# Performance work log

Measured on AMD Instinct MI355X. Metric: run time of the kernel, lower is better.

## Reference

```python
import jax, jax.numpy as jnp
import numpy as np
import math

N = 50000          # number of nodes
K = 32             # fixed neighbor-list degree
D_IN = 256
D_OUT = 256
TPERC = 0.45


def setup_inputs() -> dict:
    key = jax.random.key(0)
    k1, k2, k3 = jax.random.split(key, 3)
    x = jax.random.normal(k1, (N, D_IN), dtype=jnp.float32)
    nbrs = jax.random.randint(k2, (N, K), 0, N, dtype=jnp.int64)
    # nn.Linear weight: [out_features, in_features], scaled ~1/sqrt(fan_in)
    W = jax.random.normal(k3, (D_OUT, D_IN), dtype=jnp.float32) / np.sqrt(D_IN)
    return {"x": x, "nbrs": nbrs, "W": W}


def reference(x, nbrs, W):
    # h = Linear(x): [N, D_OUT]
    h = jnp.einsum("ni,oi->no", x, W)
    # gather neighbor messages: [N, K, D_OUT]
    msgs = h[nbrs]
    # per-node sort over the neighbor axis (feature-wise, as torch.sort(dim=0))
    msgs = jnp.sort(msgs, axis=1)
    remove = math.floor(K * TPERC)  # static trim count (14 when K=32)
    if remove > 0:
        msgs = msgs[:, remove:K - remove]
    # trimmed mean over remaining neighbors: [N, D_OUT]
    return jnp.mean(msgs, axis=1)
```

## Files before the change

kernel.cpp:

```cpp
#include <hip/hip_runtime.h>
#include <hip/hip_fp16.h>

#define D      256
#define NNODES 50000
#define KNBR   32
#define NGRP   8
#define GRPC   32

typedef _Float16 h8 __attribute__((ext_vector_type(8)));
typedef _Float16 h2 __attribute__((ext_vector_type(2)));
typedef float    f4 __attribute__((ext_vector_type(4)));

__device__ __forceinline__ h2 h2min(h2 a, h2 b) {
  h2 d; asm("v_pk_min_f16 %0, %1, %2" : "=v"(d) : "v"(a), "v"(b)); return d;
}
__device__ __forceinline__ h2 h2max(h2 a, h2 b) {
  h2 d; asm("v_pk_max_f16 %0, %1, %2" : "=v"(d) : "v"(a), "v"(b)); return d;
}

__device__ __forceinline__ void gll16(const void* g, void* l) {
  __builtin_amdgcn_global_load_lds(
      (const __attribute__((address_space(1))) void*)g,
      (__attribute__((address_space(3))) void*)l, 16, 0, 0);
}


__global__ void wcvt(const float* __restrict__ W, _Float16* __restrict__ whi,
                     _Float16* __restrict__ wlo) {
  int i = (blockIdx.x * 256 + threadIdx.x) * 4;
  float4 w = *(const float4*)&W[i];
  float wf[4] = {w.x, w.y, w.z, w.w};
  union { _Float16 h[4]; uint2 u; } H, L;
#pragma unroll
  for (int e = 0; e < 4; e++) {
    _Float16 hi = (_Float16)wf[e];
    H.h[e] = hi;
    L.h[e] = (_Float16)(wf[e] - (float)hi);
  }
  *(uint2*)&whi[i] = H.u;
  *(uint2*)&wlo[i] = L.u;
}

__global__ __launch_bounds__(256, 4)
void gemm_mfma(const float* __restrict__ x, const _Float16* __restrict__ Whi,
               const _Float16* __restrict__ Wlo, _Float16* __restrict__ hblk) {
  __shared__ _Float16 Ws[2][4][256][8];

  const int tid  = threadIdx.x;
  const int lane = tid & 63;
  const int wv   = tid >> 6;
  const int wvu  = __builtin_amdgcn_readfirstlane(wv);
  const int c    = lane & 15;
  const int ko   = lane >> 4;
  const int brow = blockIdx.x * 64;

  int arow = brow + wv * 16 + c;
  if (arow >= NNODES) arow = NNODES - 1;
  const float* xrow = &x[(size_t)arow * D];

  f4 acc[16];
#pragma unroll
  for (int j = 0; j < 16; j++) acc[j] = (f4)(0.f);

  auto stage = [&](int t) {
    const int k0 = t * 32;
#pragma unroll
    for (int q = 0; q < 8; q++) {
      const int fb = wvu * 512 + q * 64;
      const int f  = fb + lane;
      const int hsel = f >> 10;
      const int kq   = (f >> 8) & 3;
      const int col  = f & 255;
      const _Float16* src = (hsel ? Wlo : Whi) + (size_t)col * D + k0 + kq * 8;
      gll16(src, (char*)Ws + (size_t)fb * 16);
    }
  };

  stage(0);
  __syncthreads();

  float4 xa0 = *(const float4*)(xrow + ko * 8);
  float4 xa1 = *(const float4*)(xrow + ko * 8 + 4);

  for (int ks = 0; ks < 8; ks++) {
    float4 xb0, xb1;
    if (ks < 7) {
      xb0 = *(const float4*)(xrow + (ks + 1) * 32 + ko * 8);
      xb1 = *(const float4*)(xrow + (ks + 1) * 32 + ko * 8 + 4);
    }

    float xf[8] = {xa0.x, xa0.y, xa0.z, xa0.w, xa1.x, xa1.y, xa1.z, xa1.w};
    h8 ahi, alo;
#pragma unroll
    for (int e = 0; e < 8; e++) {
      _Float16 hi = (_Float16)xf[e];
      ahi[e] = hi;
      alo[e] = (_Float16)(xf[e] - (float)hi);
    }

#pragma unroll
    for (int j = 0; j < 16; j++) {
      h8 bhi = *(const h8*)&Ws[0][ko][j * 16 + c][0];
      h8 blo = *(const h8*)&Ws[1][ko][j * 16 + c][0];
      acc[j] = __builtin_amdgcn_mfma_f32_16x16x32_f16(ahi, bhi, acc[j], 0, 0, 0);
      acc[j] = __builtin_amdgcn_mfma_f32_16x16x32_f16(ahi, blo, acc[j], 0, 0, 0);
      acc[j] = __builtin_amdgcn_mfma_f32_16x16x32_f16(alo, bhi, acc[j], 0, 0, 0);
    }

    if (ks < 7) {
      __syncthreads();
      stage(ks + 1);
      __syncthreads();
      xa0 = xb0; xa1 = xb1;
    }
  }

#pragma unroll
  for (int j = 0; j < 16; j++) {
    const int g  = j >> 1;
    const int oc = (j & 1) * 16 + c;
#pragma unroll
    for (int r = 0; r < 4; r++) {
      const int n = brow + wv * 16 + ko * 4 + r;
      if (n < NNODES)
        hblk[((size_t)g * NNODES + n) * GRPC + oc] = (_Float16)acc[j][r];
    }
  }
}

template <int P, int K>
__device__ __forceinline__ void oem_pass(h2* v) {
#pragma unroll
  for (int j = K % P; j + K < 32; j += 2 * K) {
#pragma unroll
    for (int i = 0; i < K; i++) {
      if (i + j + K < 32 && ((i + j) / (2 * P) == (i + j + K) / (2 * P))) {
        h2 lo = h2min(v[i + j], v[i + j + K]);
        h2 hi = h2max(v[i + j], v[i + j + K]);
        v[i + j] = lo;
        v[i + j + K] = hi;
      }
    }
  }
}

__device__ __forceinline__ void sort32(h2* v) {
  oem_pass<1, 1>(v);
  oem_pass<2, 2>(v);  oem_pass<2, 1>(v);
  oem_pass<4, 4>(v);  oem_pass<4, 2>(v);  oem_pass<4, 1>(v);
  oem_pass<8, 8>(v);  oem_pass<8, 4>(v);  oem_pass<8, 2>(v);  oem_pass<8, 1>(v);
  oem_pass<16, 16>(v); oem_pass<16, 8>(v); oem_pass<16, 4>(v);
  oem_pass<16, 2>(v);  oem_pass<16, 1>(v);
}

__global__ __launch_bounds__(256, 4)
void trimmed_gather(const _Float16* __restrict__ hblk, const int* __restrict__ nbrs,
                    float* __restrict__ out) {
  __shared__ int nb[16 * KNBR];
  const int bid   = blockIdx.x;
  const int g     = bid & 7;
  const int chunk = bid >> 3;
  const int n0    = chunk * 16;
  const int t     = threadIdx.x;

  nb[t]       = nbrs[n0 * KNBR + t];
  nb[t + 256] = nbrs[n0 * KNBR + 256 + t];
  __syncthreads();

  const int nl = t >> 4;
  const int cp = t & 15;
  const size_t gbase = (size_t)g * NNODES * GRPC;

  h2 v[KNBR];
#pragma unroll
  for (int k = 0; k < KNBR; k++) {
    const int r = nb[nl * KNBR + k];
    v[k] = *(const h2*)&hblk[gbase + (size_t)r * GRPC + cp * 2];
  }

  sort32(v);

  float2 res;
  res.x = ((float)v[14][0] + (float)v[15][0] + (float)v[16][0] + (float)v[17][0]) * 0.25f;
  res.y = ((float)v[14][1] + (float)v[15][1] + (float)v[16][1] + (float)v[17][1]) * 0.25f;

  const int n = n0 + nl;
  *(float2*)&out[(size_t)n * D + g * GRPC + cp * 2] = res;
}

extern "C" void kernel_launch(void* const* d_in, const int* in_sizes, int n_in,
                              void* d_out, int out_size, void* d_ws, size_t ws_size,
                              hipStream_t stream) {
  const float* x    = (const float*)d_in[0];
  const int*   nbrs = (const int*)d_in[1];
  const float* W    = (const float*)d_in[2];
  float*       out  = (float*)d_out;

  _Float16* hblk = (_Float16*)d_ws;
  _Float16* Whi  = (_Float16*)((char*)d_ws + 25600000);
  _Float16* Wlo  = Whi + 65536;

  wcvt<<<dim3(64), dim3(256), 0, stream>>>(W, Whi, Wlo);
  gemm_mfma<<<dim3((NNODES + 63) / 64), dim3(256), 0, stream>>>(x, Whi, Wlo, hblk);
  trimmed_gather<<<dim3(NGRP * (NNODES / 16)), dim3(256), 0, stream>>>(
      hblk, nbrs, out);
}
```

Measured before the change: 223.3 us.

## Drop W low-part correction, retile GEMM, and replace full sort with median-4 selection

The GEMM now splits only x into hi/lo fp16 parts and drops the W low-part term, cutting MFMA count by a third. It also uses 128x128 tiles on a 2D grid with double-buffered LDS staging, which removes one barrier per k-step. The gather kernel handles 4 channels per thread with 8-byte loads and 32 nodes per block. It replaces the full 32-element sorting network with two 16-sorts plus a partial merge that extracts only the middle four elements. Dropping the W correction lowers precision of the linear layer, and the wider per-thread state raises register pressure.

```diff
diff --git a/kernel.cpp b/kernel.cpp
--- a/kernel.cpp
+++ b/kernel.cpp
@@ -8,6 +8,7 @@
 #define GRPC   32
 
 typedef _Float16 h8 __attribute__((ext_vector_type(8)));
+typedef _Float16 h4 __attribute__((ext_vector_type(4)));
 typedef _Float16 h2 __attribute__((ext_vector_type(2)));
 typedef float    f4 __attribute__((ext_vector_type(4)));
 
@@ -25,26 +26,19 @@
 }
 
 
-__global__ void wcvt(const float* __restrict__ W, _Float16* __restrict__ whi,
-                     _Float16* __restrict__ wlo) {
+__global__ void wcvt(const float* __restrict__ W, _Float16* __restrict__ whi) {
   int i = (blockIdx.x * 256 + threadIdx.x) * 4;
   float4 w = *(const float4*)&W[i];
-  float wf[4] = {w.x, w.y, w.z, w.w};
-  union { _Float16 h[4]; uint2 u; } H, L;
-#pragma unroll
-  for (int e = 0; e < 4; e++) {
-    _Float16 hi = (_Float16)wf[e];
-    H.h[e] = hi;
-    L.h[e] = (_Float16)(wf[e] - (float)hi);
-  }
+  union { _Float16 h[4]; uint2 u; } H;
+  H.h[0] = (_Float16)w.x; H.h[1] = (_Float16)w.y;
+  H.h[2] = (_Float16)w.z; H.h[3] = (_Float16)w.w;
   *(uint2*)&whi[i] = H.u;
-  *(uint2*)&wlo[i] = L.u;
 }
 
 __global__ __launch_bounds__(256, 4)
 void gemm_mfma(const float* __restrict__ x, const _Float16* __restrict__ Whi,
-               const _Float16* __restrict__ Wlo, _Float16* __restrict__ hblk) {
-  __shared__ _Float16 Ws[2][4][256][8];
+               _Float16* __restrict__ hblk) {
+  __shared__ _Float16 Ws[2][4][128][8];
 
   const int tid  = threadIdx.x;
   const int lane = tid & 63;
@@ -52,89 +46,109 @@
   const int wvu  = __builtin_amdgcn_readfirstlane(wv);
   const int c    = lane & 15;
   const int ko   = lane >> 4;
-  const int brow = blockIdx.x * 64;
-
-  int arow = brow + wv * 16 + c;
-  if (arow >= NNODES) arow = NNODES - 1;
-  const float* xrow = &x[(size_t)arow * D];
-
-  f4 acc[16];
-#pragma unroll
-  for (int j = 0; j < 16; j++) acc[j] = (f4)(0.f);
-
-  auto stage = [&](int t) {
+  const int brow = blockIdx.x * 128;
+  const int bcol = blockIdx.y * 128;
+
+  const float* xrow[2];
+#pragma unroll
+  for (int tl = 0; tl < 2; tl++) {
+    int ar = brow + wv * 32 + tl * 16 + c;
+    if (ar >= NNODES) ar = NNODES - 1;
+    xrow[tl] = &x[(size_t)ar * D];
+  }
+
+  f4 acc[2][8];
+#pragma unroll
+  for (int tl = 0; tl < 2; tl++)
+#pragma unroll
+    for (int j = 0; j < 8; j++) acc[tl][j] = (f4)(0.f);
+
+  auto stage = [&](int buf, int t) {
     const int k0 = t * 32;
 #pragma unroll
-    for (int q = 0; q < 8; q++) {
-      const int fb = wvu * 512 + q * 64;
-      const int f  = fb + lane;
-      const int hsel = f >> 10;
-      const int kq   = (f >> 8) & 3;
-      const int col  = f & 255;
-      const _Float16* src = (hsel ? Wlo : Whi) + (size_t)col * D + k0 + kq * 8;
-      gll16(src, (char*)Ws + (size_t)fb * 16);
+    for (int q = 0; q < 2; q++) {
+      const int fb   = wvu * 128 + q * 64;
+      const int f    = fb + lane;
+      const int kq   = f >> 7;
+      const int colL = f & 127;
+      gll16(&Whi[(size_t)(bcol + colL) * D + k0 + kq * 8],
+            (char*)Ws + ((size_t)buf * 512 + fb) * 16);
     }
   };
 
-  stage(0);
+  stage(0, 0);
   __syncthreads();
 
-  float4 xa0 = *(const float4*)(xrow + ko * 8);
-  float4 xa1 = *(const float4*)(xrow + ko * 8 + 4);
-
-  for (int ks = 0; ks < 8; ks++) {
-    float4 xb0, xb1;
-    if (ks < 7) {
-      xb0 = *(const float4*)(xrow + (ks + 1) * 32 + ko * 8);
-      xb1 = *(const float4*)(xrow + (ks + 1) * 32 + ko * 8 + 4);
-    }
-
-    float xf[8] = {xa0.x, xa0.y, xa0.z, xa0.w, xa1.x, xa1.y, xa1.z, xa1.w};
-    h8 ahi, alo;
-#pragma unroll
-    for (int e = 0; e < 8; e++) {
-      _Float16 hi = (_Float16)xf[e];
-      ahi[e] = hi;
-      alo[e] = (_Float16)(xf[e] - (float)hi);
-    }
-
-#pragma unroll
-    for (int j = 0; j < 16; j++) {
-      h8 bhi = *(const h8*)&Ws[0][ko][j * 16 + c][0];
-      h8 blo = *(const h8*)&Ws[1][ko][j * 16 + c][0];
-      acc[j] = __builtin_amdgcn_mfma_f32_16x16x32_f16(ahi, bhi, acc[j], 0, 0, 0);
-      acc[j] = __builtin_amdgcn_mfma_f32_16x16x32_f16(ahi, blo, acc[j], 0, 0, 0);
-      acc[j] = __builtin_amdgcn_mfma_f32_16x16x32_f16(alo, bhi, acc[j], 0, 0, 0);
-    }
-
-    if (ks < 7) {
+  float4 xa[2][2], xb[2][2];
+#pragma unroll
+  for (int tl = 0; tl < 2; tl++) {
+    xa[tl][0] = *(const float4*)(xrow[tl] + ko * 8);
+    xa[tl][1] = *(const float4*)(xrow[tl] + ko * 8 + 4);
+  }
+
+  for (int t = 0; t < 8; ++t) {
+    const int buf = t & 1;
+    if (t < 7) {
+      stage(buf ^ 1, t + 1);
+#pragma unroll
+      for (int tl = 0; tl < 2; tl++) {
+        xb[tl][0] = *(const float4*)(xrow[tl] + (t + 1) * 32 + ko * 8);
+        xb[tl][1] = *(const float4*)(xrow[tl] + (t + 1) * 32 + ko * 8 + 4);
+      }
+    }
+
+    h8 ahi[2], alo[2];
+#pragma unroll
+    for (int tl = 0; tl < 2; tl++) {
+      float xf[8] = {xa[tl][0].x, xa[tl][0].y, xa[tl][0].z, xa[tl][0].w,
+                     xa[tl][1].x, xa[tl][1].y, xa[tl][1].z, xa[tl][1].w};
+#pragma unroll
+      for (int e = 0; e < 8; e++) {
+        _Float16 hi = (_Float16)xf[e];
+        ahi[tl][e] = hi;
+        alo[tl][e] = (_Float16)(xf[e] - (float)hi);
+      }
+    }
+
+#pragma unroll
+    for (int j = 0; j < 8; j++) {
+      h8 bhi = *(const h8*)&Ws[buf][ko][j * 16 + c][0];
+#pragma unroll
+      for (int tl = 0; tl < 2; tl++) {
+        acc[tl][j] = __builtin_amdgcn_mfma_f32_16x16x32_f16(ahi[tl], bhi, acc[tl][j], 0, 0, 0);
+        acc[tl][j] = __builtin_amdgcn_mfma_f32_16x16x32_f16(alo[tl], bhi, acc[tl][j], 0, 0, 0);
+      }
+    }
+
+    if (t < 7) {
       __syncthreads();
-      stage(ks + 1);
-      __syncthreads();
-      xa0 = xb0; xa1 = xb1;
-    }
-  }
-
-#pragma unroll
-  for (int j = 0; j < 16; j++) {
-    const int g  = j >> 1;
-    const int oc = (j & 1) * 16 + c;
-#pragma unroll
-    for (int r = 0; r < 4; r++) {
-      const int n = brow + wv * 16 + ko * 4 + r;
-      if (n < NNODES)
-        hblk[((size_t)g * NNODES + n) * GRPC + oc] = (_Float16)acc[j][r];
-    }
-  }
-}
-
-template <int P, int K>
+#pragma unroll
+      for (int tl = 0; tl < 2; tl++) { xa[tl][0] = xb[tl][0]; xa[tl][1] = xb[tl][1]; }
+    }
+  }
+
+#pragma unroll
+  for (int tl = 0; tl < 2; tl++)
+#pragma unroll
+    for (int j = 0; j < 8; j++) {
+      const int g  = (bcol >> 5) + (j >> 1);
+      const int oc = (j & 1) * 16 + c;
+#pragma unroll
+      for (int r = 0; r < 4; r++) {
+        const int n = brow + wv * 32 + tl * 16 + ko * 4 + r;
+        if (n < NNODES)
+          hblk[((size_t)g * NNODES + n) * GRPC + oc] = (_Float16)acc[tl][j][r];
+      }
+    }
+}
+
+template <int N, int P, int K>
 __device__ __forceinline__ void oem_pass(h2* v) {
 #pragma unroll
-  for (int j = K % P; j + K < 32; j += 2 * K) {
+  for (int j = K % P; j + K < N; j += 2 * K) {
 #pragma unroll
     for (int i = 0; i < K; i++) {
-      if (i + j + K < 32 && ((i + j) / (2 * P) == (i + j + K) / (2 * P))) {
+      if (i + j + K < N && ((i + j) / (2 * P) == (i + j + K) / (2 * P))) {
         h2 lo = h2min(v[i + j], v[i + j + K]);
         h2 hi = h2max(v[i + j], v[i + j + K]);
         v[i + j] = lo;
@@ -144,48 +158,80 @@
   }
 }
 
-__device__ __forceinline__ void sort32(h2* v) {
-  oem_pass<1, 1>(v);
-  oem_pass<2, 2>(v);  oem_pass<2, 1>(v);
-  oem_pass<4, 4>(v);  oem_pass<4, 2>(v);  oem_pass<4, 1>(v);
-  oem_pass<8, 8>(v);  oem_pass<8, 4>(v);  oem_pass<8, 2>(v);  oem_pass<8, 1>(v);
-  oem_pass<16, 16>(v); oem_pass<16, 8>(v); oem_pass<16, 4>(v);
-  oem_pass<16, 2>(v);  oem_pass<16, 1>(v);
+__device__ __forceinline__ void sort16(h2* v) {
+  oem_pass<16, 1, 1>(v);
+  oem_pass<16, 2, 2>(v);  oem_pass<16, 2, 1>(v);
+  oem_pass<16, 4, 4>(v);  oem_pass<16, 4, 2>(v);  oem_pass<16, 4, 1>(v);
+  oem_pass<16, 8, 8>(v);  oem_pass<16, 8, 4>(v);  oem_pass<16, 8, 2>(v);
+  oem_pass<16, 8, 1>(v);
+}
+
+__device__ __forceinline__ void ce(h2* v, int a, int b) {
+  h2 lo = h2min(v[a], v[b]);
+  h2 hi = h2max(v[a], v[b]);
+  v[a] = lo; v[b] = hi;
+}
+
+__device__ __forceinline__ void select_mid4(h2* v) {
+  sort16(v);
+  sort16(v + 16);
+#pragma unroll
+  for (int i = 0; i < 16; i++) ce(v, i, 31 - i);
+#pragma unroll
+  for (int i = 0; i < 8; i++) ce(v, i, i + 8);
+#pragma unroll
+  for (int i = 8; i < 12; i++) ce(v, i, i + 4);
+  ce(v, 12, 14); ce(v, 13, 15);
+#pragma unroll
+  for (int i = 16; i < 24; i++) ce(v, i, i + 8);
+#pragma unroll
+  for (int i = 16; i < 20; i++) ce(v, i, i + 4);
+  ce(v, 16, 18); ce(v, 17, 19);
 }
 
 __global__ __launch_bounds__(256, 4)
 void trimmed_gather(const _Float16* __restrict__ hblk, const int* __restrict__ nbrs,
                     float* __restrict__ out) {
-  __shared__ int nb[16 * KNBR];
+  __shared__ int nb[32 * KNBR];
   const int bid   = blockIdx.x;
   const int g     = bid & 7;
   const int chunk = bid >> 3;
-  const int n0    = chunk * 16;
+  const int n0    = chunk * 32;
   const int t     = threadIdx.x;
 
-  nb[t]       = nbrs[n0 * KNBR + t];
-  nb[t + 256] = nbrs[n0 * KNBR + 256 + t];
+#pragma unroll
+  for (int q = 0; q < 4; q++) {
+    int idx = n0 * KNBR + q * 256 + t;
+    if (idx >= NNODES * KNBR) idx = NNODES * KNBR - 1;
+    nb[q * 256 + t] = nbrs[idx];
+  }
   __syncthreads();
 
-  const int nl = t >> 4;
-  const int cp = t & 15;
-  const size_t gbase = (size_t)g * NNODES * GRPC;
-
-  h2 v[KNBR];
+  const int nl = t >> 3;
+  const int cp = t & 7;
+  const _Float16* base = hblk + (size_t)g * NNODES * GRPC + cp * 4;
+
+  h2 va[KNBR], vb[KNBR];
 #pragma unroll
   for (int k = 0; k < KNBR; k++) {
     const int r = nb[nl * KNBR + k];
-    v[k] = *(const h2*)&hblk[gbase + (size_t)r * GRPC + cp * 2];
-  }
-
-  sort32(v);
-
-  float2 res;
-  res.x = ((float)v[14][0] + (float)v[15][0] + (float)v[16][0] + (float)v[17][0]) * 0.25f;
-  res.y = ((float)v[14][1] + (float)v[15][1] + (float)v[16][1] + (float)v[17][1]) * 0.25f;
+    h4 w = *(const h4*)(base + (size_t)r * GRPC);
+    va[k] = __builtin_shufflevector(w, w, 0, 1);
+    vb[k] = __builtin_shufflevector(w, w, 2, 3);
+  }
+
+  select_mid4(va);
+  select_mid4(vb);
+
+  float4 res;
+  res.x = ((float)va[14][0] + (float)va[15][0] + (float)va[16][0] + (float)va[17][0]) * 0.25f;
+  res.y = ((float)va[14][1] + (float)va[15][1] + (float)va[16][1] + (float)va[17][1]) * 0.25f;
+  res.z = ((float)vb[14][0] + (float)vb[15][0] + (float)vb[16][0] + (float)vb[17][0]) * 0.25f;
+  res.w = ((float)vb[14][1] + (float)vb[15][1] + (float)vb[16][1] + (float)vb[17][1]) * 0.25f;
 
   const int n = n0 + nl;
-  *(float2*)&out[(size_t)n * D + g * GRPC + cp * 2] = res;
+  if (n < NNODES)
+    *(float4*)&out[(size_t)n * D + g * GRPC + cp * 4] = res;
 }
 
 extern "C" void kernel_launch(void* const* d_in, const int* in_sizes, int n_in,
@@ -198,10 +244,9 @@
 
   _Float16* hblk = (_Float16*)d_ws;
   _Float16* Whi  = (_Float16*)((char*)d_ws + 25600000);
-  _Float16* Wlo  = Whi + 65536;
-
-  wcvt<<<dim3(64), dim3(256), 0, stream>>>(W, Whi, Wlo);
-  gemm_mfma<<<dim3((NNODES + 63) / 64), dim3(256), 0, stream>>>(x, Whi, Wlo, hblk);
-  trimmed_gather<<<dim3(NGRP * (NNODES / 16)), dim3(256), 0, stream>>>(
+
+  wcvt<<<dim3(64), dim3(256), 0, stream>>>(W, Whi);
+  gemm_mfma<<<dim3((NNODES + 127) / 128, 2), dim3(256), 0, stream>>>(x, Whi, hblk);
+  trimmed_gather<<<dim3(NGRP * ((NNODES + 31) / 32)), dim3(256), 0, stream>>>(
       hblk, nbrs, out);
 }
```

Measured after the change: 205.4 us. -8.0%, faster.
